# Kernel optimization log

Measured on AMD Instinct MI355X. Metric: run time of the kernel, lower is better.

The kernel has to match this reference:

```python
import jax, jax.numpy as jnp
import numpy as np

N = 50000
E = 800000
IN_C = 128
HID = 128
EMB = 128
OUT_C = 40
BN_EPS = 1e-5


def setup_inputs() -> dict:
    key = jax.random.key(0)
    ks = jax.random.split(key, 24)
    inp = {}
    inp['x'] = jax.random.normal(ks[0], (N, IN_C), dtype=jnp.float32)
    inp['edge_index'] = jax.random.randint(ks[1], (2, E), 0, N, dtype=jnp.int32)
    # GCNConv weights (PyG GCNConv: out = norm_agg(x @ W) + b)
    dims = [(IN_C, HID), (HID, HID), (HID, HID + EMB)]
    for i, (fi, fo) in enumerate(dims, 1):
        inp[f'conv_w{i}'] = jax.random.normal(ks[2 * i], (fi, fo), dtype=jnp.float32) / np.sqrt(fi)
        inp[f'conv_b{i}'] = jnp.zeros((fo,), dtype=jnp.float32)
        # BatchNorm (eval mode: running stats)
        inp[f'bn_g{i}'] = jax.random.uniform(ks[2 * i + 1], (fo,), minval=0.5, maxval=1.5, dtype=jnp.float32)
        inp[f'bn_b{i}'] = jax.random.normal(jax.random.fold_in(ks[2 * i + 1], 1), (fo,), dtype=jnp.float32) * 0.1
        inp[f'bn_m{i}'] = jax.random.normal(jax.random.fold_in(ks[2 * i + 1], 2), (fo,), dtype=jnp.float32) * 0.1
        inp[f'bn_v{i}'] = jax.random.uniform(jax.random.fold_in(ks[2 * i + 1], 3), (fo,), minval=0.5, maxval=1.5, dtype=jnp.float32)
    inp['lin_w1'] = jax.random.normal(ks[20], (HID + EMB, HID), dtype=jnp.float32) / np.sqrt(HID + EMB)
    inp['lin_b1'] = jnp.zeros((HID,), dtype=jnp.float32)
    inp['lin_w2'] = jax.random.normal(ks[21], (HID, OUT_C), dtype=jnp.float32) / np.sqrt(HID)
    inp['lin_b2'] = jnp.zeros((OUT_C,), dtype=jnp.float32)
    return inp


def _gcn_norm(edge_index, n):
    # add self-loops, symmetric normalization D^-1/2 (A+I) D^-1/2
    loops = jnp.arange(n, dtype=edge_index.dtype)
    src = jnp.concatenate([edge_index[0], loops])
    dst = jnp.concatenate([edge_index[1], loops])
    deg = jax.ops.segment_sum(jnp.ones_like(dst, dtype=jnp.float32), dst, num_segments=n)
    dinv = jax.lax.rsqrt(jnp.maximum(deg, 1.0))
    norm = dinv[src] * dinv[dst]
    return src, dst, norm


def _gcn_layer(x, w, b, src, dst, norm, n):
    xw = x @ w                      # [N, Fo] dense GEMM
    msg = xw[src] * norm[:, None]   # [E+N, Fo] gather + scale
    out = jax.ops.segment_sum(msg, dst, num_segments=n)  # scatter-add
    return out + b


def _bn_eval(h, g, b, m, v):
    return (h - m) * jax.lax.rsqrt(v + BN_EPS) * g + b


def reference(x, edge_index,
              conv_w1, conv_b1, bn_g1, bn_b1, bn_m1, bn_v1,
              conv_w2, conv_b2, bn_g2, bn_b2, bn_m2, bn_v2,
              conv_w3, conv_b3, bn_g3, bn_b3, bn_m3, bn_v3,
              lin_w1, lin_b1, lin_w2, lin_b2):
    n = x.shape[0]
    src, dst, norm = _gcn_norm(edge_index, n)
    convs = [(conv_w1, conv_b1, bn_g1, bn_b1, bn_m1, bn_v1),
             (conv_w2, conv_b2, bn_g2, bn_b2, bn_m2, bn_v2),
             (conv_w3, conv_b3, bn_g3, bn_b3, bn_m3, bn_v3)]
    h = x
    for (w, b, g, bb, m, v) in convs:
        h = _gcn_layer(h, w, b, src, dst, norm, n)
        h = jax.nn.relu(_bn_eval(h, g, bb, m, v))
        # dropout: identity (eval mode)
    h = jax.nn.relu(h @ lin_w1 + lin_b1)
    return h @ lin_w2 + lin_b2
```

## Files before the change

### kernel.cpp

```cpp
#include <hip/hip_runtime.h>
#include <hip/hip_fp16.h>


typedef _Float16 f16x8 __attribute__((ext_vector_type(8)));
typedef float f32x4 __attribute__((ext_vector_type(4)));

static inline int cdiv(int a, int b) { return (a + b - 1) / b; }

__global__ __launch_bounds__(256) void k_zero_int(int* p, int n) {
    int i = blockIdx.x * 256 + threadIdx.x;
    if (i < n) p[i] = 0;
}

__global__ __launch_bounds__(256) void k_bcount(const int* __restrict__ ei, int E,
                                                int* bucketCount, int* blockBase) {
    __shared__ int lh[256];
    lh[threadIdx.x] = 0;
    __syncthreads();
    int base = blockIdx.x * 2048;
#pragma unroll
    for (int i = 0; i < 8; ++i) {
        int e = base + i * 256 + threadIdx.x;
        if (e < E) atomicAdd(&lh[ei[E + e] >> 8], 1);
    }
    __syncthreads();
    blockBase[blockIdx.x * 256 + threadIdx.x] =
        atomicAdd(&bucketCount[threadIdx.x], lh[threadIdx.x]);
}

__global__ void k_bscan(const int* __restrict__ bucketCount, int* bucketPtr, int nbk,
                        int* rowptr, int N, int E) {
    __shared__ int s[1024];
    int v = (threadIdx.x < nbk) ? bucketCount[threadIdx.x] : 0;
    s[threadIdx.x] = v;
    __syncthreads();
    for (int off = 1; off < 1024; off <<= 1) {
        int t = (threadIdx.x >= (unsigned)off) ? s[threadIdx.x - off] : 0;
        __syncthreads();
        s[threadIdx.x] += t;
        __syncthreads();
    }
    if (threadIdx.x < nbk) bucketPtr[threadIdx.x] = s[threadIdx.x] - v;
    if (threadIdx.x == 0) {
        bucketPtr[nbk] = E;
        rowptr[N] = E;
    }
}

__global__ __launch_bounds__(256) void k_bscatter(const int* __restrict__ ei, int E,
                                                  const int* __restrict__ bucketPtr,
                                                  const int* __restrict__ blockBase,
                                                  unsigned int* __restrict__ ebuf) {
    __shared__ int lh[256];
    lh[threadIdx.x] = 0;
    __syncthreads();
    int base = blockIdx.x * 2048;
    const int* bb = &blockBase[blockIdx.x * 256];
#pragma unroll
    for (int i = 0; i < 8; ++i) {
        int e = base + i * 256 + threadIdx.x;
        if (e < E) {
            unsigned int src = (unsigned int)ei[e];
            unsigned int dst = (unsigned int)ei[E + e];
            int b = dst >> 8;
            int lp = atomicAdd(&lh[b], 1);
            ebuf[bucketPtr[b] + bb[b] + lp] = src | ((dst & 255u) << 24);
        }
    }
}

__global__ __launch_bounds__(256) void k_bcsr(const unsigned int* __restrict__ ebuf,
                                              const int* __restrict__ bucketPtr,
                                              int* __restrict__ rowptr, float* __restrict__ dinv,
                                              int* __restrict__ csr, int N) {
    __shared__ int hist[256], excl[256], cur[256];
    const int b = blockIdx.x;
    const int base = bucketPtr[b];
    const int cnt = bucketPtr[b + 1] - base;
    const int t = threadIdx.x;
    hist[t] = 0;
    cur[t] = 0;
    __syncthreads();
    for (int i = t; i < cnt; i += 256) atomicAdd(&hist[ebuf[base + i] >> 24], 1);
    __syncthreads();
    int v = hist[t];
    excl[t] = v;
    __syncthreads();
    for (int off = 1; off < 256; off <<= 1) {
        int x = (t >= off) ? excl[t - off] : 0;
        __syncthreads();
        excl[t] += x;
        __syncthreads();
    }
    int ex = excl[t] - v;
    int node = b * 256 + t;
    if (node < N) {
        rowptr[node] = base + ex;
        dinv[node] = rsqrtf((float)(v + 1));
    }
    __syncthreads();
    excl[t] = ex;
    __syncthreads();
    for (int i = t; i < cnt; i += 256) {
        unsigned int e = ebuf[base + i];
        int ln = e >> 24;
        int pos = base + excl[ln] + atomicAdd(&cur[ln], 1);
        csr[pos] = (int)(e & 0xFFFFFFu);
    }
}

__device__ inline bool wt_job(int i, int lo, int hi, int K, int FO, const float* W, __half* T) {
    if (i < lo || i >= hi) return false;
    int j = i - lo;
    int c = j / K;
    int k = j - c * K;
    T[j] = (c < FO) ? __float2half_rn(W[(size_t)k * FO + c]) : __half(0.f);
    return true;
}

__global__ __launch_bounds__(256) void k_prep(const float* __restrict__ x, __half* __restrict__ XH,
                                              int nf,
                                              const float* w1, const float* w2, const float* w3,
                                              const float* w4, const float* w5, __half* t1,
                                              __half* t2, __half* t3, __half* t4, __half* t5) {
    int i = blockIdx.x * 256 + threadIdx.x;
    if (i < nf) {
        float4 v = ((const float4*)x)[i];
        __half h[4] = {__float2half_rn(v.x), __float2half_rn(v.y), __float2half_rn(v.z),
                       __float2half_rn(v.w)};
        ((uint2*)XH)[i] = *(uint2*)h;
        return;
    }
    int j = i - nf;
    if (wt_job(j, 0, 16384, 128, 128, w1, t1)) return;
    if (wt_job(j, 16384, 32768, 128, 128, w2, t2)) return;
    if (wt_job(j, 32768, 65536, 128, 256, w3, t3)) return;
    if (wt_job(j, 65536, 98304, 256, 128, w4, t4)) return;
    wt_job(j, 98304, 106496, 128, 40, w5, t5);
}

__global__ __launch_bounds__(256) void k_gather64(const int* __restrict__ rowptr,
                                                  const int* __restrict__ csr,
                                                  const float* __restrict__ dinv,
                                                  const __half* __restrict__ xh,
                                                  __half* __restrict__ G, int N) {
    int t = blockIdx.x * 256 + threadIdx.x;
    int node = t >> 6;
    if (node >= N) return;
    int lane = t & 63;
    const __half2* xb = (const __half2*)xh;
    float di = dinv[node];
    float ax = 0.f, ay = 0.f;
    int p0 = rowptr[node], p1 = rowptr[node + 1];
    int p = p0;
    for (; p + 8 <= p1; p += 8) {
        int s_[8];
        float wg[8];
        __half2 v[8];
#pragma unroll
        for (int j = 0; j < 8; ++j) s_[j] = csr[p + j];
#pragma unroll
        for (int j = 0; j < 8; ++j) wg[j] = dinv[s_[j]];
#pragma unroll
        for (int j = 0; j < 8; ++j) v[j] = xb[(size_t)s_[j] * 64 + lane];
#pragma unroll
        for (int j = 0; j < 8; ++j) {
            float2 f = __half22float2(v[j]);
            ax += wg[j] * f.x;
            ay += wg[j] * f.y;
        }
    }
    for (; p + 4 <= p1; p += 4) {
        int s_[4];
        float wg[4];
        __half2 v[4];
#pragma unroll
        for (int j = 0; j < 4; ++j) s_[j] = csr[p + j];
#pragma unroll
        for (int j = 0; j < 4; ++j) wg[j] = dinv[s_[j]];
#pragma unroll
        for (int j = 0; j < 4; ++j) v[j] = xb[(size_t)s_[j] * 64 + lane];
#pragma unroll
        for (int j = 0; j < 4; ++j) {
            float2 f = __half22float2(v[j]);
            ax += wg[j] * f.x;
            ay += wg[j] * f.y;
        }
    }
    for (; p < p1; ++p) {
        int src = csr[p];
        float w = dinv[src];
        float2 f = __half22float2(xb[(size_t)src * 64 + lane]);
        ax += w * f.x;
        ay += w * f.y;
    }
    {
        float2 f = __half22float2(xb[(size_t)node * 64 + lane]);
        ax = di * (ax + di * f.x);
        ay = di * (ay + di * f.y);
    }
    ((__half2*)G)[(size_t)node * 64 + lane] = __floats2half2_rn(ax, ay);
}

template <int K, bool BN, bool RELU, typename OT>
__global__ __launch_bounds__(256) void k_mfma(const __half* __restrict__ A,
                                              const __half* __restrict__ Wt,
                                              const float* __restrict__ cb,
                                              const float* __restrict__ g,
                                              const float* __restrict__ bb,
                                              const float* __restrict__ m,
                                              const float* __restrict__ vv,
                                              OT* __restrict__ Y, int ldy, int N, int ncols) {
    constexpr int KS = K / 32;
    constexpr int NCT = 4;
    __shared__ __half bs[KS * NCT * 64 * 8];

    const int tid = threadIdx.x;
    const int col0 = blockIdx.y * 64;

    constexpr int PIECES = KS * NCT * 64;
#pragma unroll
    for (int p = tid; p < PIECES; p += 256) {
        int ks = p / (NCT * 64);
        int rem = p - ks * (NCT * 64);
        int ct = rem >> 6;
        int l = rem & 63;
        int col = col0 + ct * 16 + (l & 15);
        int kg = ks * 32 + (l >> 4) * 8;
        *(uint4*)&bs[p * 8] = *(const uint4*)&Wt[(size_t)col * K + kg];
    }
    __syncthreads();

    const int wave = tid >> 6;
    const int lane = tid & 63;
    const int rbase = blockIdx.x * 128 + wave * 32;
    const int r0 = rbase + (lane & 15);
    const int k0 = (lane >> 4) * 8;

    uint4 af[2][KS];
#pragma unroll
    for (int ks = 0; ks < KS; ++ks) {
        int kk = ks * 32 + k0;
        af[0][ks] = (r0 < N) ? *(const uint4*)&A[(size_t)r0 * K + kk] : uint4{0, 0, 0, 0};
        af[1][ks] = (r0 + 16 < N) ? *(const uint4*)&A[(size_t)(r0 + 16) * K + kk]
                                  : uint4{0, 0, 0, 0};
    }

    f32x4 acc[2][NCT];
#pragma unroll
    for (int rt = 0; rt < 2; ++rt)
#pragma unroll
        for (int ct = 0; ct < NCT; ++ct) acc[rt][ct] = {0.f, 0.f, 0.f, 0.f};

#pragma unroll
    for (int ks = 0; ks < KS; ++ks) {
        f16x8 b[NCT];
#pragma unroll
        for (int ct = 0; ct < NCT; ++ct)
            b[ct] = *(const f16x8*)&bs[((ks * NCT + ct) * 64 + lane) * 8];
#pragma unroll
        for (int rt = 0; rt < 2; ++rt) {
            f16x8 a = *(const f16x8*)&af[rt][ks];
#pragma unroll
            for (int ct = 0; ct < NCT; ++ct)
                acc[rt][ct] = __builtin_amdgcn_mfma_f32_16x16x32_f16(a, b[ct], acc[rt][ct], 0, 0, 0);
        }
    }

    const int cbase = col0 + (lane & 15);
#pragma unroll
    for (int ct = 0; ct < NCT; ++ct) {
        int col = cbase + ct * 16;
        if (col >= ncols) continue;
        float sc, sh;
        if (BN) {
            sc = g[col] * rsqrtf(vv[col] + 1e-5f);
            sh = bb[col] + (cb[col] - m[col]) * sc;
        } else {
            sc = 1.f;
            sh = cb[col];
        }
#pragma unroll
        for (int rt = 0; rt < 2; ++rt) {
#pragma unroll
            for (int r = 0; r < 4; ++r) {
                int row = rbase + rt * 16 + (lane >> 4) * 4 + r;
                if (row < N) {
                    float o = acc[rt][ct][r] * sc + sh;
                    if (RELU) o = fmaxf(o, 0.f);
                    if constexpr (sizeof(OT) == 2) {
                        Y[(size_t)row * ldy + col] = __float2half_rn(o);
                    } else {
                        Y[(size_t)row * ldy + col] = o;
                    }
                }
            }
        }
    }
}

extern "C" void kernel_launch(void* const* d_in, const int* in_sizes, int n_in,
                              void* d_out, int out_size, void* d_ws, size_t ws_size,
                              hipStream_t stream) {
    const float* x = (const float*)d_in[0];
    const int* ei = (const int*)d_in[1];
    const float* cw1 = (const float*)d_in[2];
    const float* cb1 = (const float*)d_in[3];
    const float* g1 = (const float*)d_in[4];
    const float* bb1 = (const float*)d_in[5];
    const float* m1 = (const float*)d_in[6];
    const float* v1 = (const float*)d_in[7];
    const float* cw2 = (const float*)d_in[8];
    const float* cb2 = (const float*)d_in[9];
    const float* g2 = (const float*)d_in[10];
    const float* bb2 = (const float*)d_in[11];
    const float* m2 = (const float*)d_in[12];
    const float* v2 = (const float*)d_in[13];
    const float* cw3 = (const float*)d_in[14];
    const float* cb3 = (const float*)d_in[15];
    const float* g3 = (const float*)d_in[16];
    const float* bb3 = (const float*)d_in[17];
    const float* m3 = (const float*)d_in[18];
    const float* v3 = (const float*)d_in[19];
    const float* lw1 = (const float*)d_in[20];
    const float* lb1 = (const float*)d_in[21];
    const float* lw2 = (const float*)d_in[22];
    const float* lb2 = (const float*)d_in[23];
    float* out = (float*)d_out;

    const int N = in_sizes[0] / 128;
    const int E = in_sizes[1] / 2;
    const int NBK = cdiv(N, 256);
    const int NBA = cdiv(E, 2048);

    auto al = [](size_t v) { return (v + 255) & ~(size_t)255; };
    char* w = (char*)d_ws;
    size_t o = 0;
    float* dinv  = (float*)(w + o);  o = al(o + (size_t)N * 4);
    int* rowptr  = (int*)(w + o);    o = al(o + (size_t)(N + 1) * 4);
    int* bcount  = (int*)(w + o);    o = al(o + 256 * 4);
    int* bptr    = (int*)(w + o);    o = al(o + (256 + 1) * 4);
    int* bbase   = (int*)(w + o);    o = al(o + (size_t)NBA * 256 * 4);
    unsigned int* ebuf = (unsigned int*)(w + o); o = al(o + (size_t)E * 4);
    int* csr     = (int*)(w + o);    o = al(o + (size_t)E * 4);
    __half* XH   = (__half*)(w + o); o = al(o + (size_t)N * 128 * 2);
    __half* GH   = (__half*)(w + o); o = al(o + (size_t)N * 128 * 2);
    __half* H3h  = (__half*)(w + o); o = al(o + (size_t)N * 256 * 2);
    __half* Wt1  = (__half*)(w + o); o = al(o + (size_t)128 * 128 * 2);
    __half* Wt2  = (__half*)(w + o); o = al(o + (size_t)128 * 128 * 2);
    __half* Wt3  = (__half*)(w + o); o = al(o + (size_t)256 * 128 * 2);
    __half* Wt4  = (__half*)(w + o); o = al(o + (size_t)128 * 256 * 2);
    __half* Wt5  = (__half*)(w + o); o = al(o + (size_t)64 * 128 * 2);
    __half* Zh   = GH;

    k_zero_int<<<1, 256, 0, stream>>>(bcount, 256);
    k_bcount<<<NBA, 256, 0, stream>>>(ei, E, bcount, bbase);
    k_bscan<<<1, 1024, 0, stream>>>(bcount, bptr, NBK, rowptr, N, E);
    k_bscatter<<<NBA, 256, 0, stream>>>(ei, E, bptr, bbase, ebuf);
    k_bcsr<<<NBK, 256, 0, stream>>>(ebuf, bptr, rowptr, dinv, csr, N);

    k_prep<<<cdiv(N * 32 + 106496, 256), 256, 0, stream>>>(x, XH, N * 32, cw1, cw2, cw3, lw1,
                                                           lw2, Wt1, Wt2, Wt3, Wt4, Wt5);

    const int gx = cdiv(N, 128);

    k_gather64<<<cdiv(N, 4), 256, 0, stream>>>(rowptr, csr, dinv, XH, GH, N);
    k_mfma<128, true, true, __half><<<dim3(gx, 2), 256, 0, stream>>>(
        GH, Wt1, cb1, g1, bb1, m1, v1, XH, 128, N, 128);
    k_gather64<<<cdiv(N, 4), 256, 0, stream>>>(rowptr, csr, dinv, XH, GH, N);
    k_mfma<128, true, true, __half><<<dim3(gx, 2), 256, 0, stream>>>(
        GH, Wt2, cb2, g2, bb2, m2, v2, XH, 128, N, 128);
    k_gather64<<<cdiv(N, 4), 256, 0, stream>>>(rowptr, csr, dinv, XH, GH, N);
    k_mfma<128, true, true, __half><<<dim3(gx, 4), 256, 0, stream>>>(
        GH, Wt3, cb3, g3, bb3, m3, v3, H3h, 256, N, 256);
    k_mfma<256, false, true, __half><<<dim3(gx, 2), 256, 0, stream>>>(
        H3h, Wt4, lb1, nullptr, nullptr, nullptr, nullptr, Zh, 128, N, 128);
    k_mfma<128, false, false, float><<<dim3(gx, 1), 256, 0, stream>>>(
        Zh, Wt5, lb2, nullptr, nullptr, nullptr, nullptr, out, 40, N, 40);
}
```

Before: 227.9 us.

## Merge graph preprocessing kernels and fold bucket scan into consumers

The bucket-count kernel is merged with the x/weight fp16 conversion into one launch. The single-block bucket scan kernel is removed, and each scatter and CSR block now recomputes the 256-entry prefix sum in shared memory. The zero kernel becomes a hipMemsetAsync. This cuts the number of kernel launches and serial dependencies in the front-end, at the cost of redundant small scans per block. The scan now assumes NBK <= 256, which holds for N = 50000.

```diff
diff --git a/kernel.cpp b/kernel.cpp
--- a/kernel.cpp
+++ b/kernel.cpp
@@ -6,108 +6,6 @@
 typedef float f32x4 __attribute__((ext_vector_type(4)));
 
 static inline int cdiv(int a, int b) { return (a + b - 1) / b; }
-
-__global__ __launch_bounds__(256) void k_zero_int(int* p, int n) {
-    int i = blockIdx.x * 256 + threadIdx.x;
-    if (i < n) p[i] = 0;
-}
-
-__global__ __launch_bounds__(256) void k_bcount(const int* __restrict__ ei, int E,
-                                                int* bucketCount, int* blockBase) {
-    __shared__ int lh[256];
-    lh[threadIdx.x] = 0;
-    __syncthreads();
-    int base = blockIdx.x * 2048;
-#pragma unroll
-    for (int i = 0; i < 8; ++i) {
-        int e = base + i * 256 + threadIdx.x;
-        if (e < E) atomicAdd(&lh[ei[E + e] >> 8], 1);
-    }
-    __syncthreads();
-    blockBase[blockIdx.x * 256 + threadIdx.x] =
-        atomicAdd(&bucketCount[threadIdx.x], lh[threadIdx.x]);
-}
-
-__global__ void k_bscan(const int* __restrict__ bucketCount, int* bucketPtr, int nbk,
-                        int* rowptr, int N, int E) {
-    __shared__ int s[1024];
-    int v = (threadIdx.x < nbk) ? bucketCount[threadIdx.x] : 0;
-    s[threadIdx.x] = v;
-    __syncthreads();
-    for (int off = 1; off < 1024; off <<= 1) {
-        int t = (threadIdx.x >= (unsigned)off) ? s[threadIdx.x - off] : 0;
-        __syncthreads();
-        s[threadIdx.x] += t;
-        __syncthreads();
-    }
-    if (threadIdx.x < nbk) bucketPtr[threadIdx.x] = s[threadIdx.x] - v;
-    if (threadIdx.x == 0) {
-        bucketPtr[nbk] = E;
-        rowptr[N] = E;
-    }
-}
-
-__global__ __launch_bounds__(256) void k_bscatter(const int* __restrict__ ei, int E,
-                                                  const int* __restrict__ bucketPtr,
-                                                  const int* __restrict__ blockBase,
-                                                  unsigned int* __restrict__ ebuf) {
-    __shared__ int lh[256];
-    lh[threadIdx.x] = 0;
-    __syncthreads();
-    int base = blockIdx.x * 2048;
-    const int* bb = &blockBase[blockIdx.x * 256];
-#pragma unroll
-    for (int i = 0; i < 8; ++i) {
-        int e = base + i * 256 + threadIdx.x;
-        if (e < E) {
-            unsigned int src = (unsigned int)ei[e];
-            unsigned int dst = (unsigned int)ei[E + e];
-            int b = dst >> 8;
-            int lp = atomicAdd(&lh[b], 1);
-            ebuf[bucketPtr[b] + bb[b] + lp] = src | ((dst & 255u) << 24);
-        }
-    }
-}
-
-__global__ __launch_bounds__(256) void k_bcsr(const unsigned int* __restrict__ ebuf,
-                                              const int* __restrict__ bucketPtr,
-                                              int* __restrict__ rowptr, float* __restrict__ dinv,
-                                              int* __restrict__ csr, int N) {
-    __shared__ int hist[256], excl[256], cur[256];
-    const int b = blockIdx.x;
-    const int base = bucketPtr[b];
-    const int cnt = bucketPtr[b + 1] - base;
-    const int t = threadIdx.x;
-    hist[t] = 0;
-    cur[t] = 0;
-    __syncthreads();
-    for (int i = t; i < cnt; i += 256) atomicAdd(&hist[ebuf[base + i] >> 24], 1);
-    __syncthreads();
-    int v = hist[t];
-    excl[t] = v;
-    __syncthreads();
-    for (int off = 1; off < 256; off <<= 1) {
-        int x = (t >= off) ? excl[t - off] : 0;
-        __syncthreads();
-        excl[t] += x;
-        __syncthreads();
-    }
-    int ex = excl[t] - v;
-    int node = b * 256 + t;
-    if (node < N) {
-        rowptr[node] = base + ex;
-        dinv[node] = rsqrtf((float)(v + 1));
-    }
-    __syncthreads();
-    excl[t] = ex;
-    __syncthreads();
-    for (int i = t; i < cnt; i += 256) {
-        unsigned int e = ebuf[base + i];
-        int ln = e >> 24;
-        int pos = base + excl[ln] + atomicAdd(&cur[ln], 1);
-        csr[pos] = (int)(e & 0xFFFFFFu);
-    }
-}
 
 __device__ inline bool wt_job(int i, int lo, int hi, int K, int FO, const float* W, __half* T) {
     if (i < lo || i >= hi) return false;
@@ -118,12 +16,29 @@
     return true;
 }
 
-__global__ __launch_bounds__(256) void k_prep(const float* __restrict__ x, __half* __restrict__ XH,
-                                              int nf,
-                                              const float* w1, const float* w2, const float* w3,
-                                              const float* w4, const float* w5, __half* t1,
-                                              __half* t2, __half* t3, __half* t4, __half* t5) {
-    int i = blockIdx.x * 256 + threadIdx.x;
+__global__ __launch_bounds__(256) void k_front(const int* __restrict__ ei, int E, int NBA,
+                                               int* bucketCount, int* blockBase,
+                                               const float* __restrict__ x,
+                                               __half* __restrict__ XH, int nf,
+                                               const float* w1, const float* w2, const float* w3,
+                                               const float* w4, const float* w5, __half* t1,
+                                               __half* t2, __half* t3, __half* t4, __half* t5) {
+    __shared__ int lh[256];
+    if ((int)blockIdx.x < NBA) {
+        lh[threadIdx.x] = 0;
+        __syncthreads();
+        int base = blockIdx.x * 2048;
+#pragma unroll
+        for (int i = 0; i < 8; ++i) {
+            int e = base + i * 256 + threadIdx.x;
+            if (e < E) atomicAdd(&lh[ei[E + e] >> 8], 1);
+        }
+        __syncthreads();
+        blockBase[blockIdx.x * 256 + threadIdx.x] =
+            atomicAdd(&bucketCount[threadIdx.x], lh[threadIdx.x]);
+        return;
+    }
+    int i = (blockIdx.x - NBA) * 256 + threadIdx.x;
     if (i < nf) {
         float4 v = ((const float4*)x)[i];
         __half h[4] = {__float2half_rn(v.x), __float2half_rn(v.y), __float2half_rn(v.z),
@@ -137,6 +52,92 @@
     if (wt_job(j, 32768, 65536, 128, 256, w3, t3)) return;
     if (wt_job(j, 65536, 98304, 256, 128, w4, t4)) return;
     wt_job(j, 98304, 106496, 128, 40, w5, t5);
+}
+
+__global__ __launch_bounds__(256) void k_bscatter(const int* __restrict__ ei, int E,
+                                                  const int* __restrict__ bcount,
+                                                  const int* __restrict__ blockBase,
+                                                  unsigned int* __restrict__ ebuf) {
+    __shared__ int sc[256];
+    __shared__ int bp[256];
+    __shared__ int lh[256];
+    const int t = threadIdx.x;
+    int v = bcount[t];
+    sc[t] = v;
+    __syncthreads();
+    for (int off = 1; off < 256; off <<= 1) {
+        int x = (t >= off) ? sc[t - off] : 0;
+        __syncthreads();
+        sc[t] += x;
+        __syncthreads();
+    }
+    bp[t] = sc[t] - v;
+    lh[t] = 0;
+    __syncthreads();
+    int base = blockIdx.x * 2048;
+    const int* bb = &blockBase[blockIdx.x * 256];
+#pragma unroll
+    for (int i = 0; i < 8; ++i) {
+        int e = base + i * 256 + t;
+        if (e < E) {
+            unsigned int src = (unsigned int)ei[e];
+            unsigned int dst = (unsigned int)ei[E + e];
+            int b = dst >> 8;
+            int lp = atomicAdd(&lh[b], 1);
+            ebuf[bp[b] + bb[b] + lp] = src | ((dst & 255u) << 24);
+        }
+    }
+}
+
+__global__ __launch_bounds__(256) void k_bcsr(const unsigned int* __restrict__ ebuf,
+                                              const int* __restrict__ bcount,
+                                              int* __restrict__ rowptr, float* __restrict__ dinv,
+                                              int* __restrict__ csr, int N, int E) {
+    __shared__ int sc[256];
+    __shared__ int hist[256], excl[256], cur[256];
+    const int b = blockIdx.x;
+    const int t = threadIdx.x;
+    int bv = bcount[t];
+    sc[t] = bv;
+    __syncthreads();
+    for (int off = 1; off < 256; off <<= 1) {
+        int x = (t >= off) ? sc[t - off] : 0;
+        __syncthreads();
+        sc[t] += x;
+        __syncthreads();
+    }
+    const int cnt = bcount[b];
+    const int base = sc[b] - cnt;
+    if (b == (int)gridDim.x - 1 && t == 0) rowptr[N] = E;
+    hist[t] = 0;
+    cur[t] = 0;
+    __syncthreads();
+    for (int i = t; i < cnt; i += 256) atomicAdd(&hist[ebuf[base + i] >> 24], 1);
+    __syncthreads();
+    int v = hist[t];
+    excl[t] = v;
+    __syncthreads();
+    for (int off = 1; off < 256; off <<= 1) {
+        int x = (t >= off) ? excl[t - off] : 0;
+        __syncthreads();
+        excl[t] += x;
+        __syncthreads();
+    }
+    int ex = excl[t] - v;
+    int node = b * 256 + t;
+    if (node < N) {
+        rowptr[node] = base + ex;
+        dinv[node] = rsqrtf((float)(v + 1));
+    }
+    __syncthreads();
+    excl[t] = ex;
+    __syncthreads();
+    for (int i = t; i < cnt; i += 256) {
+        unsigned int e = ebuf[base + i];
+        int ln = e >> 24;
+        int pos = base + excl[ln] + atomicAdd(&cur[ln], 1);
+        csr[pos] = (int)(e & 0xFFFFFFu);
+    }
 }
 
 __global__ __launch_bounds__(256) void k_gather64(const int* __restrict__ rowptr,
@@ -339,7 +340,6 @@
     float* dinv  = (float*)(w + o);  o = al(o + (size_t)N * 4);
     int* rowptr  = (int*)(w + o);    o = al(o + (size_t)(N + 1) * 4);
     int* bcount  = (int*)(w + o);    o = al(o + 256 * 4);
-    int* bptr    = (int*)(w + o);    o = al(o + (256 + 1) * 4);
     int* bbase   = (int*)(w + o);    o = al(o + (size_t)NBA * 256 * 4);
     unsigned int* ebuf = (unsigned int*)(w + o); o = al(o + (size_t)E * 4);
     int* csr     = (int*)(w + o);    o = al(o + (size_t)E * 4);
@@ -353,14 +353,13 @@
     __half* Wt5  = (__half*)(w + o); o = al(o + (size_t)64 * 128 * 2);
     __half* Zh   = GH;
 
-    k_zero_int<<<1, 256, 0, stream>>>(bcount, 256);
-    k_bcount<<<NBA, 256, 0, stream>>>(ei, E, bcount, bbase);
-    k_bscan<<<1, 1024, 0, stream>>>(bcount, bptr, NBK, rowptr, N, E);
-    k_bscatter<<<NBA, 256, 0, stream>>>(ei, E, bptr, bbase, ebuf);
-    k_bcsr<<<NBK, 256, 0, stream>>>(ebuf, bptr, rowptr, dinv, csr, N);
-
-    k_prep<<<cdiv(N * 32 + 106496, 256), 256, 0, stream>>>(x, XH, N * 32, cw1, cw2, cw3, lw1,
-                                                           lw2, Wt1, Wt2, Wt3, Wt4, Wt5);
+    hipMemsetAsync(bcount, 0, 256 * sizeof(int), stream);
+    const int nf = N * 32;
+    const int prepBlocks = cdiv(nf + 106496, 256);
+    k_front<<<NBA + prepBlocks, 256, 0, stream>>>(ei, E, NBA, bcount, bbase, x, XH, nf, cw1, cw2,
+                                                  cw3, lw1, lw2, Wt1, Wt2, Wt3, Wt4, Wt5);
+    k_bscatter<<<NBA, 256, 0, stream>>>(ei, E, bcount, bbase, ebuf);
+    k_bcsr<<<NBK, 256, 0, stream>>>(ebuf, bcount, rowptr, dinv, csr, N, E);
 
     const int gx = cdiv(N, 128);
 
```

New measurement: 222.8 us. -2.2%, faster.
